# Optimization experiments

Hardware: AMD Instinct MI355X
Metric: run time of the kernel (lower is better)

## Reference

```python
import jax, jax.numpy as jnp
import numpy as np

B, W_DIM, CIN, COUT, K, H = 16, 512, 512, 512, 3, 64
PAD = (K - 1) // 2          # conv padding, also filtered_lrelu padding
GAIN = float(np.sqrt(2.0))  # lrelu gain (not torgb)
SLOPE = 0.2                 # lrelu slope (not torgb)
CLAMP = 256.0               # conv_clamp
AFFINE_WG = float(1.0 / np.sqrt(W_DIM))  # FullyConnectedLayer weight_gain


def setup_inputs() -> dict:
    key = jax.random.key(0)
    k0, k1, k2, k3 = jax.random.split(key, 4)
    return {
        "x": jax.random.normal(k0, (B, CIN, H, H), jnp.float32),
        "w": jax.random.normal(k1, (B, W_DIM), jnp.float32),
        "affine_weight": jax.random.normal(k2, (CIN, W_DIM), jnp.float32),
        "affine_bias": jnp.ones((CIN,), jnp.float32),       # bias_init=1
        "conv_weight": jax.random.normal(k3, (COUT, CIN, K, K), jnp.float32),
        "bias": jnp.zeros((COUT,), jnp.float32),
        "magnitude_ema": jnp.ones((), jnp.float32),
    }


def reference(x, w, affine_weight, affine_bias, conv_weight, bias, magnitude_ema):
    input_gain = jax.lax.rsqrt(magnitude_ema)
    # --- affine (FullyConnectedLayer, linear act, lr_mult=1) ---
    s = w @ (affine_weight * AFFINE_WG).T + affine_bias          # [B, CIN]
    # --- modulated_conv2d with demodulation (is_torgb=False) ---
    wk = conv_weight * jax.lax.rsqrt(
        jnp.mean(jnp.square(conv_weight), axis=(1, 2, 3), keepdims=True))
    s = s * jax.lax.rsqrt(jnp.mean(jnp.square(s)))
    wb = wk[None] * s[:, None, :, None, None]                    # [B,COUT,CIN,K,K]
    dcoefs = jax.lax.rsqrt(jnp.sum(jnp.square(wb), axis=(2, 3, 4)) + 1e-8)  # [B,COUT]
    wb = wb * dcoefs[:, :, None, None, None] * input_gain
    # grouped conv: groups = batch, one weight set per sample
    xg = x.reshape(1, B * CIN, H, H)
    wg = wb.reshape(B * COUT, CIN, K, K)
    y = jax.lax.conv_general_dilated(
        xg, wg, window_strides=(1, 1), padding=[(PAD, PAD), (PAD, PAD)],
        dimension_numbers=("NCHW", "OIHW", "NCHW"), feature_group_count=B)
    y = y.reshape(B, COUT, H, H)
    # --- filtered_lrelu: up=down=1, fu=fd=None (identity FIR) ---
    # => bias add, zero-pad by `padding`, lrelu * gain, clamp
    y = y + bias[:, None, None]
    y = jnp.pad(y, ((0, 0), (0, 0), (PAD, PAD), (PAD, PAD)))
    y = jnp.where(y >= 0, y, y * SLOPE) * GAIN
    y = jnp.clip(y, -CLAMP, CLAMP)                               # [B,COUT,66,66]
    return y
```

## Files before the change

kernel.cpp:

```cpp
#include <hip/hip_runtime.h>

#define B_     16
#define WDIM   512
#define CIN_   512
#define COUT_  512
#define HH     64
#define KC     32
#define NCHUNK (CIN_/KC)
#define AFFINE_WG 0.044194173824159216f
#define GAIN_  1.4142135623730951f
#define CLAMP_ 256.0f

#define WBYTES 36864
#define XBYTES 42240

typedef __attribute__((ext_vector_type(4))) float f32x4;
typedef __attribute__((ext_vector_type(8))) short bf16x8;
typedef __attribute__((ext_vector_type(8))) unsigned short u16x8;

__device__ __forceinline__ unsigned short f2bf(float f) {
    union { float f; unsigned u; } un; un.f = f;
    unsigned u = un.u;
    u += 0x7FFFu + ((u >> 16) & 1u);
    return (unsigned short)(u >> 16);
}

__device__ __forceinline__ void gl_lds16(const void* g, void* l) {
    __builtin_amdgcn_global_load_lds(
        reinterpret_cast<const __attribute__((address_space(1))) unsigned int*>(
            reinterpret_cast<uintptr_t>(g)),
        reinterpret_cast<__attribute__((address_space(3))) unsigned int*>(
            reinterpret_cast<uintptr_t>(l)),
        16, 0, 0);
}


__global__ void k_affine(const float* __restrict__ w, const float* __restrict__ aw,
                         const float* __restrict__ ab, float* __restrict__ s,
                         float* __restrict__ part) {
    const int tid = threadIdx.x;
    const int b = blockIdx.x >> 1;
    const int c = ((blockIdx.x & 1) << 8) + tid;
    const f32x4* wr = (const f32x4*)(w + (size_t)b * WDIM);
    const f32x4* ar = (const f32x4*)(aw + (size_t)c * WDIM);
    float acc = 0.f;
    #pragma unroll 4
    for (int k = 0; k < WDIM / 4; ++k) {
        f32x4 a = ar[k], bb = wr[k];
        acc += a[0]*bb[0] + a[1]*bb[1] + a[2]*bb[2] + a[3]*bb[3];
    }
    float sv = acc * AFFINE_WG + ab[c];
    s[b * CIN_ + c] = sv;
    __shared__ float red[256];
    red[tid] = sv * sv;
    __syncthreads();
    for (int off = 128; off > 0; off >>= 1) {
        if (tid < off) red[tid] += red[tid + off];
        __syncthreads();
    }
    if (tid == 0) part[blockIdx.x] = red[0];
}

__global__ void k_wnorm(const float* __restrict__ cw, float* __restrict__ alpha,
                        float* __restrict__ Q) {
    const int o = blockIdx.x;
    const int tid = threadIdx.x;
    __shared__ float qsh[512];
    __shared__ float red[256];
    __shared__ float a_sh;
    float tot = 0.f;
    #pragma unroll
    for (int half = 0; half < 2; ++half) {
        const int c = tid + half * 256;
        const float* p = cw + ((size_t)o * 512 + c) * 9;
        float qs = 0.f;
        #pragma unroll
        for (int t = 0; t < 9; ++t) { float v = p[t]; qs += v * v; }
        qsh[c] = qs; tot += qs;
    }
    red[tid] = tot; __syncthreads();
    for (int off = 128; off > 0; off >>= 1) {
        if (tid < off) red[tid] += red[tid + off];
        __syncthreads();
    }
    if (tid == 0) { a_sh = rsqrtf(red[0] * (1.0f / 4608.0f)); alpha[o] = a_sh; }
    __syncthreads();
    const float a2 = a_sh * a_sh;
    Q[(size_t)o * 512 + tid]       = a2 * qsh[tid];
    Q[(size_t)o * 512 + tid + 256] = a2 * qsh[tid + 256];
}

__global__ void k_g(const float* __restrict__ s, const float* __restrict__ part,
                    const float* __restrict__ Q, const float* __restrict__ alpha,
                    const float* __restrict__ ema, float* __restrict__ g) {
    const int tid = threadIdx.x;
    const int b = blockIdx.x >> 1;
    const int o = ((blockIdx.x & 1) << 8) + tid;
    __shared__ float rs2_sh;
    if (tid == 0) {
        float t = 0.f;
        #pragma unroll
        for (int i = 0; i < 32; ++i) t += part[i];
        rs2_sh = 8192.0f / t;
    }
    __syncthreads();
    const f32x4* sh = (const f32x4*)(s + (size_t)b * CIN_);
    const f32x4* qq = (const f32x4*)(Q + (size_t)o * CIN_);
    float d = 0.f;
    #pragma unroll 4
    for (int k = 0; k < CIN_ / 4; ++k) {
        f32x4 a = sh[k], q4 = qq[k];
        d += a[0]*a[0]*q4[0] + a[1]*a[1]*q4[1] + a[2]*a[2]*q4[2] + a[3]*a[3]*q4[3];
    }
    const float ig = rsqrtf(ema[0]);
    g[b * COUT_ + o] = alpha[o] * rsqrtf(d * rs2_sh + 1e-8f) * ig;
}

__global__ void k_wprep2(const float* __restrict__ cw, unsigned short* __restrict__ wb) {
    const int S = blockIdx.x * 256 + threadIdx.x;
    const int p    = S / 2304;
    const int srem = S - p * 2304;
    const int a    = srem * 16;
    const int tap  = a >> 12;
    const int o    = (a >> 6) & 63;
    const int c0   = ((a & 63) ^ ((o & 6) << 3)) >> 1;
    const int ot = p >> 4, cc = p & 15;
    const int og = ot * 64 + o;
    const int cg = cc * 32 + c0;
    const float* src = cw + ((size_t)og * 512 + cg) * 9 + tap;
    u16x8 v;
    #pragma unroll
    for (int j = 0; j < 8; ++j) v[j] = f2bf(src[j * 9]);
    *(u16x8*)(wb + (size_t)S * 8) = v;
}

__global__ void k_xprep2(const float* __restrict__ x, const float* __restrict__ s,
                         const float* __restrict__ part, unsigned short* __restrict__ xbf) {
    __shared__ float rs_sh;
    __shared__ char tile[8 * 4096];
    const int tid = threadIdx.x;
    if (tid == 0) {
        float t = 0.f;
        #pragma unroll
        for (int i = 0; i < 32; ++i) t += part[i];
        rs_sh = rsqrtf(t * (1.0f / 8192.0f));
    }
    __syncthreads();
    const float rs = rs_sh;
    const int blk = blockIdx.x;
    const int b  = blk >> 7;
    const int cc = (blk >> 3) & 15;
    const int rg = blk & 7;
    const int c   = tid >> 3;
    const int k8  = tid & 7;
    const float sc = s[b * CIN_ + cc * 32 + c] * rs;
    const float* src = x + (((size_t)(b * CIN_ + cc * 32 + c)) * HH + rg * 8) * HH + k8 * 8;
    #pragma unroll
    for (int row = 0; row < 8; ++row) {
        const f32x4 v0 = *(const f32x4*)(src + (size_t)row * HH);
        const f32x4 v1 = *(const f32x4*)(src + (size_t)row * HH + 4);
        #pragma unroll
        for (int q = 0; q < 8; ++q) {
            const float v = (q < 4) ? v0[q] : v1[q - 4];
            const int col = k8 * 8 + q + 1;
            const int byte = ((col * 64 + 2 * c) ^ ((col & 6) << 3)) - 64;
            *(unsigned short*)(tile + row * 4096 + byte) = f2bf(v * sc);
        }
    }
    __syncthreads();
    unsigned short* dst = xbf + ((size_t)(b * 16 + cc) * 64 + rg * 8) * 2048;
    const u16x8* tsrc = (const u16x8*)tile;
    #pragma unroll
    for (int k = 0; k < 8; ++k)
        *(u16x8*)(dst + (size_t)(tid + k * 256) * 8) = tsrc[tid + k * 256];
}

__global__ __launch_bounds__(512, 1) void k_conv4(
    const unsigned short* __restrict__ xbf, const unsigned short* __restrict__ wb,
    const float* __restrict__ g, const float* __restrict__ bias,
    float* __restrict__ out) {
    __shared__ char bufA[WBYTES + XBYTES];
    __shared__ char bufB[WBYTES + XBYTES];

    const int tid  = threadIdx.x;
    const int lane = tid & 63;
    const int wv   = tid >> 6;
    const int l15  = lane & 15;
    const int hi   = lane >> 4;

    const int orig = blockIdx.x;
    const int wg = (orig & 7) * 128 + (orig >> 3);
    const int b  = wg >> 6;
    const int ot = (wg >> 3) & 7;
    const int rt = wg & 7;
    const int h0 = rt * 8;

    const f32x4 zero4 = {0.f, 0.f, 0.f, 0.f};
    f32x4 acc[4][4];
    #pragma unroll
    for (int i = 0; i < 4; ++i)
        #pragma unroll
        for (int j = 0; j < 4; ++j) acc[i][j] = zero4;

    {
        unsigned int* x0 = (unsigned int*)(bufA + WBYTES);
        unsigned int* x1 = (unsigned int*)(bufB + WBYTES);
        for (int i = tid; i < XBYTES / 4; i += 512) { x0[i] = 0u; x1[i] = 0u; }
    }
    __syncthreads();

    const char* wsrc0 = (const char*)wb + (size_t)ot * 16 * WBYTES;
    const char* xsrc0 = (const char*)xbf + (size_t)b * 16 * 262144;

    auto STAGE = [&](char* base, int cc) {
        if (tid < 256) {
            const char* wsrc = wsrc0 + (size_t)cc * WBYTES;
            #pragma unroll
            for (int r = 0; r < 9; ++r)
                gl_lds16(wsrc + r * 4096 + tid * 16, base + r * 4096 + tid * 16);
        } else {
            const int t2 = tid - 256;
            const char* xsrc = xsrc0 + (size_t)cc * 262144;
            char* xb = base + WBYTES;
            #pragma unroll
            for (int r = 0; r < 10; ++r) {
                const int h_in = h0 - 1 + r;
                if ((unsigned)h_in < 64u)
                    gl_lds16(xsrc + (size_t)h_in * 4096 + t2 * 16,
                             xb + r * 4224 + 64 + t2 * 16);
            }
        }
    };

    auto COMPUTE = [&](const char* Wl, const char* Xl) {
        #pragma unroll
        for (int tap = 0; tap < 9; ++tap) {
            const int ti = tap / 3, tj = tap - ti * 3;
            bf16x8 af[4];
            #pragma unroll
            for (int mi = 0; mi < 4; ++mi) {
                const int o = mi * 16 + l15;
                int byte = (tap << 12) + (o << 6) + (hi << 4);
                byte ^= ((o & 6) << 3);
                af[mi] = *(const bf16x8*)(Wl + byte);
            }
            bf16x8 bg[4];
            const int row = wv + ti;
            #pragma unroll
            for (int ni = 0; ni < 4; ++ni) {
                const int col = ni * 16 + l15 + tj;
                int byte = (((row * 66 + col) << 5) + (hi << 3)) << 1;
                byte ^= ((col & 6) << 3);
                bg[ni] = *(const bf16x8*)(Xl + byte);
            }
            if (tap == 5) __builtin_amdgcn_s_barrier();
            __builtin_amdgcn_s_setprio(1);
            #pragma unroll
            for (int mi = 0; mi < 4; ++mi)
                #pragma unroll
                for (int ni = 0; ni < 4; ++ni)
                    acc[mi][ni] = __builtin_amdgcn_mfma_f32_16x16x32_bf16(
                        af[mi], bg[ni], acc[mi][ni], 0, 0, 0);
            __builtin_amdgcn_s_setprio(0);
        }
    };

    STAGE(bufA, 0);
    __syncthreads();

    #pragma unroll 1
    for (int it = 0; it < 8; ++it) {
        const int cc = it * 2;
        STAGE(bufB, cc + 1);
        COMPUTE(bufA, bufA + WBYTES);
        __syncthreads();
        if (cc + 2 < NCHUNK) STAGE(bufA, cc + 2);
        COMPUTE(bufB, bufB + WBYTES);
        __syncthreads();
    }

    {
        const int obase = ot * 64;
        const int orow = h0 + wv + 1;
        #pragma unroll
        for (int mi = 0; mi < 4; ++mi) {
            #pragma unroll
            for (int r = 0; r < 4; ++r) {
                const int o = obase + mi * 16 + hi * 4 + r;
                const float gg = g[b * COUT_ + o];
                const float bb = bias[o];
                float* op = out + ((size_t)(b * COUT_ + o) * 66 + orow) * 66;
                #pragma unroll
                for (int ni = 0; ni < 4; ++ni) {
                    float v = acc[mi][ni][r] * gg + bb;
                    v = (v >= 0.f ? v : v * 0.2f) * GAIN_;
                    v = fminf(fmaxf(v, -CLAMP_), CLAMP_);
                    op[ni * 16 + l15 + 1] = v;
                }
                if (l15 == 0)  op[0]  = 0.f;
                if (l15 == 15) op[65] = 0.f;
            }
        }
        if (rt == 0 || rt == 7) {
            const int row = (rt == 0) ? 0 : 65;
            for (int i = tid; i < 64 * 66; i += 512) {
                const int o = obase + i / 66, col = i - (i / 66) * 66;
                out[((size_t)(b * COUT_ + o) * 66 + row) * 66 + col] = 0.f;
            }
        }
    }
}

extern "C" void kernel_launch(void* const* d_in, const int* in_sizes, int n_in,
                              void* d_out, int out_size, void* d_ws, size_t ws_size,
                              hipStream_t stream) {
    const float* x    = (const float*)d_in[0];
    const float* w    = (const float*)d_in[1];
    const float* aw   = (const float*)d_in[2];
    const float* ab   = (const float*)d_in[3];
    const float* cw   = (const float*)d_in[4];
    const float* bias = (const float*)d_in[5];
    const float* ema  = (const float*)d_in[6];
    float* out = (float*)d_out;

    float* wsf   = (float*)d_ws;
    float* s     = wsf;
    float* part  = wsf + 8192;
    float* alpha = wsf + 16512;
    float* Q     = wsf + 17024;
    float* g     = wsf + 279168;
    unsigned short* wb  = (unsigned short*)((char*)d_ws + 1179648);
    unsigned short* xbf = (unsigned short*)((char*)d_ws + 5898240);

    k_affine <<<32, 256, 0, stream>>>(w, aw, ab, s, part);
    k_wnorm  <<<512, 256, 0, stream>>>(cw, alpha, Q);
    k_g      <<<32, 256, 0, stream>>>(s, part, Q, alpha, ema, g);
    k_wprep2 <<<1152, 256, 0, stream>>>(cw, wb);
    k_xprep2 <<<2048, 256, 0, stream>>>(x, s, part, xbf);
    k_conv4  <<<1024, 512, 0, stream>>>(xbf, wb, g, bias, out);
}
```

Before: 342.1 us.

## Replace double-buffered 512-thread conv with single-buffer 256-thread, 2-blocks-per-CU conv

The conv kernel moves from 512 threads with two LDS buffers and software double-buffering to 256 threads with a single LDS buffer and two output rows per wave. The intent is to run two blocks per CU so that one block's loads overlap with the other's MFMA work, in place of the explicit intra-block pipeline, while also reusing each loaded weight fragment across two rows. The cost is twice the accumulator registers per thread (128 floats of acc) and the loss of explicit prefetch. Load-to-compute overlap now depends on the other block sharing the CU.

```diff
diff --git a/kernel.cpp b/kernel.cpp
--- a/kernel.cpp
+++ b/kernel.cpp
@@ -175,12 +175,12 @@
         *(u16x8*)(dst + (size_t)(tid + k * 256) * 8) = tsrc[tid + k * 256];
 }
 
-__global__ __launch_bounds__(512, 1) void k_conv4(
+__global__ __launch_bounds__(256, 2) void k_conv5(
     const unsigned short* __restrict__ xbf, const unsigned short* __restrict__ wb,
     const float* __restrict__ g, const float* __restrict__ bias,
     float* __restrict__ out) {
-    __shared__ char bufA[WBYTES + XBYTES];
-    __shared__ char bufB[WBYTES + XBYTES];
+    __shared__ char Wl[WBYTES];
+    __shared__ char Xl[XBYTES];
 
     const int tid  = threadIdx.x;
     const int lane = tid & 63;
@@ -196,43 +196,41 @@
     const int h0 = rt * 8;
 
     const f32x4 zero4 = {0.f, 0.f, 0.f, 0.f};
-    f32x4 acc[4][4];
-    #pragma unroll
-    for (int i = 0; i < 4; ++i)
-        #pragma unroll
-        for (int j = 0; j < 4; ++j) acc[i][j] = zero4;
+    f32x4 acc[2][4][4];
+    #pragma unroll
+    for (int rr = 0; rr < 2; ++rr)
+        #pragma unroll
+        for (int i = 0; i < 4; ++i)
+            #pragma unroll
+            for (int j = 0; j < 4; ++j) acc[rr][i][j] = zero4;
 
     {
-        unsigned int* x0 = (unsigned int*)(bufA + WBYTES);
-        unsigned int* x1 = (unsigned int*)(bufB + WBYTES);
-        for (int i = tid; i < XBYTES / 4; i += 512) { x0[i] = 0u; x1[i] = 0u; }
+        unsigned int* x0 = (unsigned int*)Xl;
+        for (int i = tid; i < XBYTES / 4; i += 256) x0[i] = 0u;
     }
     __syncthreads();
 
     const char* wsrc0 = (const char*)wb + (size_t)ot * 16 * WBYTES;
     const char* xsrc0 = (const char*)xbf + (size_t)b * 16 * 262144;
 
-    auto STAGE = [&](char* base, int cc) {
-        if (tid < 256) {
+    #pragma unroll 1
+    for (int cc = 0; cc < NCHUNK; ++cc) {
+        {
             const char* wsrc = wsrc0 + (size_t)cc * WBYTES;
             #pragma unroll
             for (int r = 0; r < 9; ++r)
-                gl_lds16(wsrc + r * 4096 + tid * 16, base + r * 4096 + tid * 16);
-        } else {
-            const int t2 = tid - 256;
+                gl_lds16(wsrc + r * 4096 + tid * 16, Wl + r * 4096 + tid * 16);
             const char* xsrc = xsrc0 + (size_t)cc * 262144;
-            char* xb = base + WBYTES;
             #pragma unroll
             for (int r = 0; r < 10; ++r) {
                 const int h_in = h0 - 1 + r;
                 if ((unsigned)h_in < 64u)
-                    gl_lds16(xsrc + (size_t)h_in * 4096 + t2 * 16,
-                             xb + r * 4224 + 64 + t2 * 16);
-            }
-        }
-    };
-
-    auto COMPUTE = [&](const char* Wl, const char* Xl) {
+                    gl_lds16(xsrc + (size_t)h_in * 4096 + tid * 16,
+                             Xl + r * 4224 + 64 + tid * 16);
+            }
+        }
+        __syncthreads();
+
         #pragma unroll
         for (int tap = 0; tap < 9; ++tap) {
             const int ti = tap / 3, tj = tap - ti * 3;
@@ -244,66 +242,60 @@
                 byte ^= ((o & 6) << 3);
                 af[mi] = *(const bf16x8*)(Wl + byte);
             }
-            bf16x8 bg[4];
-            const int row = wv + ti;
-            #pragma unroll
-            for (int ni = 0; ni < 4; ++ni) {
-                const int col = ni * 16 + l15 + tj;
-                int byte = (((row * 66 + col) << 5) + (hi << 3)) << 1;
-                byte ^= ((col & 6) << 3);
-                bg[ni] = *(const bf16x8*)(Xl + byte);
-            }
-            if (tap == 5) __builtin_amdgcn_s_barrier();
+            bf16x8 bg[2][4];
+            #pragma unroll
+            for (int rr = 0; rr < 2; ++rr) {
+                const int row = 2 * wv + rr + ti;
+                #pragma unroll
+                for (int ni = 0; ni < 4; ++ni) {
+                    const int col = ni * 16 + l15 + tj;
+                    int byte = (((row * 66 + col) << 5) + (hi << 3)) << 1;
+                    byte ^= ((col & 6) << 3);
+                    bg[rr][ni] = *(const bf16x8*)(Xl + byte);
+                }
+            }
             __builtin_amdgcn_s_setprio(1);
             #pragma unroll
-            for (int mi = 0; mi < 4; ++mi)
+            for (int rr = 0; rr < 2; ++rr)
                 #pragma unroll
-                for (int ni = 0; ni < 4; ++ni)
-                    acc[mi][ni] = __builtin_amdgcn_mfma_f32_16x16x32_bf16(
-                        af[mi], bg[ni], acc[mi][ni], 0, 0, 0);
+                for (int mi = 0; mi < 4; ++mi)
+                    #pragma unroll
+                    for (int ni = 0; ni < 4; ++ni)
+                        acc[rr][mi][ni] = __builtin_amdgcn_mfma_f32_16x16x32_bf16(
+                            af[mi], bg[rr][ni], acc[rr][mi][ni], 0, 0, 0);
             __builtin_amdgcn_s_setprio(0);
         }
-    };
-
-    STAGE(bufA, 0);
-    __syncthreads();
-
-    #pragma unroll 1
-    for (int it = 0; it < 8; ++it) {
-        const int cc = it * 2;
-        STAGE(bufB, cc + 1);
-        COMPUTE(bufA, bufA + WBYTES);
-        __syncthreads();
-        if (cc + 2 < NCHUNK) STAGE(bufA, cc + 2);
-        COMPUTE(bufB, bufB + WBYTES);
-        __syncthreads();
+        if (cc != NCHUNK - 1) __syncthreads();
     }
 
     {
         const int obase = ot * 64;
-        const int orow = h0 + wv + 1;
-        #pragma unroll
-        for (int mi = 0; mi < 4; ++mi) {
-            #pragma unroll
-            for (int r = 0; r < 4; ++r) {
-                const int o = obase + mi * 16 + hi * 4 + r;
-                const float gg = g[b * COUT_ + o];
-                const float bb = bias[o];
-                float* op = out + ((size_t)(b * COUT_ + o) * 66 + orow) * 66;
+        #pragma unroll
+        for (int rr = 0; rr < 2; ++rr) {
+            const int orow = h0 + 2 * wv + rr + 1;
+            #pragma unroll
+            for (int mi = 0; mi < 4; ++mi) {
                 #pragma unroll
-                for (int ni = 0; ni < 4; ++ni) {
-                    float v = acc[mi][ni][r] * gg + bb;
-                    v = (v >= 0.f ? v : v * 0.2f) * GAIN_;
-                    v = fminf(fmaxf(v, -CLAMP_), CLAMP_);
-                    op[ni * 16 + l15 + 1] = v;
+                for (int r = 0; r < 4; ++r) {
+                    const int o = obase + mi * 16 + hi * 4 + r;
+                    const float gg = g[b * COUT_ + o];
+                    const float bb = bias[o];
+                    float* op = out + ((size_t)(b * COUT_ + o) * 66 + orow) * 66;
+                    #pragma unroll
+                    for (int ni = 0; ni < 4; ++ni) {
+                        float v = acc[rr][mi][ni][r] * gg + bb;
+                        v = (v >= 0.f ? v : v * 0.2f) * GAIN_;
+                        v = fminf(fmaxf(v, -CLAMP_), CLAMP_);
+                        op[ni * 16 + l15 + 1] = v;
+                    }
+                    if (l15 == 0)  op[0]  = 0.f;
+                    if (l15 == 15) op[65] = 0.f;
                 }
-                if (l15 == 0)  op[0]  = 0.f;
-                if (l15 == 15) op[65] = 0.f;
             }
         }
         if (rt == 0 || rt == 7) {
             const int row = (rt == 0) ? 0 : 65;
-            for (int i = tid; i < 64 * 66; i += 512) {
+            for (int i = tid; i < 64 * 66; i += 256) {
                 const int o = obase + i / 66, col = i - (i / 66) * 66;
                 out[((size_t)(b * COUT_ + o) * 66 + row) * 66 + col] = 0.f;
             }
@@ -337,5 +329,5 @@
     k_g      <<<32, 256, 0, stream>>>(s, part, Q, alpha, ema, g);
     k_wprep2 <<<1152, 256, 0, stream>>>(cw, wb);
     k_xprep2 <<<2048, 256, 0, stream>>>(x, s, part, xbf);
-    k_conv4  <<<1024, 512, 0, stream>>>(xbf, wb, g, bias, out);
-}
+    k_conv5  <<<1024, 256, 0, stream>>>(xbf, wb, g, bias, out);
+}
```

After: 337.7 us. Within noise of the previous version (-1.3%).

## Use counted vmcnt waits with explicit barriers in conv double-buffer pipeline

Applied to the files above, without the earlier changes.

The conv kernel's staging loop now has each thread issue the same number of global-to-LDS loads every stage, sending out-of-range halo rows to a dump buffer. That fixed count lets it wait with a counted s_waitcnt vmcnt instead of a full drain, so the next chunk's loads stay in flight while the current chunk is computed. Full __syncthreads are replaced by raw s_barrier calls fenced with sched_barrier, and the mid-compute barrier is removed. The cost is extra wasted loads for boundary rows, plus fragile hand-tuned wait counts that depend on how many loads each wave issues.

```diff
diff --git a/kernel.cpp b/kernel.cpp
--- a/kernel.cpp
+++ b/kernel.cpp
@@ -13,6 +13,7 @@
 
 #define WBYTES 36864
 #define XBYTES 42240
+#define BUFBYTES (WBYTES + XBYTES)
 
 typedef __attribute__((ext_vector_type(4))) float f32x4;
 typedef __attribute__((ext_vector_type(8))) short bf16x8;
@@ -175,12 +176,13 @@
         *(u16x8*)(dst + (size_t)(tid + k * 256) * 8) = tsrc[tid + k * 256];
 }
 
-__global__ __launch_bounds__(512, 1) void k_conv4(
+__global__ __launch_bounds__(512, 1) void k_conv7(
     const unsigned short* __restrict__ xbf, const unsigned short* __restrict__ wb,
     const float* __restrict__ g, const float* __restrict__ bias,
     float* __restrict__ out) {
-    __shared__ char bufA[WBYTES + XBYTES];
-    __shared__ char bufB[WBYTES + XBYTES];
+    __shared__ char bufA[BUFBYTES];
+    __shared__ char bufB[BUFBYTES];
+    __shared__ char dump[4096];
 
     const int tid  = threadIdx.x;
     const int lane = tid & 63;
@@ -225,11 +227,32 @@
             #pragma unroll
             for (int r = 0; r < 10; ++r) {
                 const int h_in = h0 - 1 + r;
-                if ((unsigned)h_in < 64u)
-                    gl_lds16(xsrc + (size_t)h_in * 4096 + t2 * 16,
-                             xb + r * 4224 + 64 + t2 * 16);
-            }
-        }
+                const bool ok = (unsigned)h_in < 64u;
+                const int hc = ok ? h_in : 0;
+                char* dst = ok ? (xb + r * 4224 + 64 + t2 * 16) : (dump + t2 * 16);
+                gl_lds16(xsrc + (size_t)hc * 4096 + t2 * 16, dst);
+            }
+        }
+    };
+
+    auto WAIT_PREV_BAR = [&]() {
+        if (wv < 4) asm volatile("s_waitcnt vmcnt(9)" ::: "memory");
+        else        asm volatile("s_waitcnt vmcnt(10)" ::: "memory");
+        __builtin_amdgcn_sched_barrier(0);
+        __builtin_amdgcn_s_barrier();
+        __builtin_amdgcn_sched_barrier(0);
+    };
+    auto WAIT0_BAR = [&]() {
+        asm volatile("s_waitcnt vmcnt(0)" ::: "memory");
+        __builtin_amdgcn_sched_barrier(0);
+        __builtin_amdgcn_s_barrier();
+        __builtin_amdgcn_sched_barrier(0);
+    };
+    auto POST_BAR = [&]() {
+        asm volatile("" ::: "memory");
+        __builtin_amdgcn_sched_barrier(0);
+        __builtin_amdgcn_s_barrier();
+        __builtin_amdgcn_sched_barrier(0);
     };
 
     auto COMPUTE = [&](const char* Wl, const char* Xl) {
@@ -253,7 +276,6 @@
                 byte ^= ((col & 6) << 3);
                 bg[ni] = *(const bf16x8*)(Xl + byte);
             }
-            if (tap == 5) __builtin_amdgcn_s_barrier();
             __builtin_amdgcn_s_setprio(1);
             #pragma unroll
             for (int mi = 0; mi < 4; ++mi)
@@ -266,18 +288,26 @@
     };
 
     STAGE(bufA, 0);
-    __syncthreads();
+    WAIT0_BAR();
 
     #pragma unroll 1
-    for (int it = 0; it < 8; ++it) {
+    for (int it = 0; it < 7; ++it) {
         const int cc = it * 2;
         STAGE(bufB, cc + 1);
+        WAIT_PREV_BAR();
         COMPUTE(bufA, bufA + WBYTES);
-        __syncthreads();
-        if (cc + 2 < NCHUNK) STAGE(bufA, cc + 2);
+        POST_BAR();
+        STAGE(bufA, cc + 2);
+        WAIT_PREV_BAR();
         COMPUTE(bufB, bufB + WBYTES);
-        __syncthreads();
-    }
+        POST_BAR();
+    }
+    STAGE(bufB, 15);
+    WAIT_PREV_BAR();
+    COMPUTE(bufA, bufA + WBYTES);
+    POST_BAR();
+    WAIT0_BAR();
+    COMPUTE(bufB, bufB + WBYTES);
 
     {
         const int obase = ot * 64;
@@ -337,5 +367,5 @@
     k_g      <<<32, 256, 0, stream>>>(s, part, Q, alpha, ema, g);
     k_wprep2 <<<1152, 256, 0, stream>>>(cw, wb);
     k_xprep2 <<<2048, 256, 0, stream>>>(x, s, part, xbf);
-    k_conv4  <<<1024, 512, 0, stream>>>(xbf, wb, g, bias, out);
-}
+    k_conv7  <<<1024, 512, 0, stream>>>(xbf, wb, g, bias, out);
+}
```

Result: slower. 349.5 us (+2.2%).

## Single-buffer conv LDS staging to raise occupancy to multiple blocks per CU

Applied to the files above, without the earlier changes.

Replaces the double-buffered LDS pipeline in the conv kernel with a single W/X buffer that is loaded, synchronised and then computed once per channel chunk. Launch bounds move from 1 to 4 blocks per CU. The goal is to roughly halve LDS use so more blocks fit per CU and other blocks hide load latency, in place of in-block prefetch overlap. The cost is that each block now stalls on every chunk's global loads, and register pressure under the tighter launch bounds may cause spills.

```diff
diff --git a/kernel.cpp b/kernel.cpp
--- a/kernel.cpp
+++ b/kernel.cpp
@@ -12,7 +12,8 @@
 #define CLAMP_ 256.0f
 
 #define WBYTES 36864
-#define XBYTES 42240
+#define XROWB  4224
+#define XBYTES (10 * XROWB)
 
 typedef __attribute__((ext_vector_type(4))) float f32x4;
 typedef __attribute__((ext_vector_type(8))) short bf16x8;
@@ -175,12 +176,12 @@
         *(u16x8*)(dst + (size_t)(tid + k * 256) * 8) = tsrc[tid + k * 256];
 }
 
-__global__ __launch_bounds__(512, 1) void k_conv4(
+__global__ __launch_bounds__(512, 4) void k_conv9(
     const unsigned short* __restrict__ xbf, const unsigned short* __restrict__ wb,
     const float* __restrict__ g, const float* __restrict__ bias,
     float* __restrict__ out) {
-    __shared__ char bufA[WBYTES + XBYTES];
-    __shared__ char bufB[WBYTES + XBYTES];
+    __shared__ char Wl[WBYTES];
+    __shared__ char Xl[XBYTES];
 
     const int tid  = threadIdx.x;
     const int lane = tid & 63;
@@ -203,36 +204,34 @@
         for (int j = 0; j < 4; ++j) acc[i][j] = zero4;
 
     {
-        unsigned int* x0 = (unsigned int*)(bufA + WBYTES);
-        unsigned int* x1 = (unsigned int*)(bufB + WBYTES);
-        for (int i = tid; i < XBYTES / 4; i += 512) { x0[i] = 0u; x1[i] = 0u; }
+        unsigned int* x0 = (unsigned int*)Xl;
+        for (int i = tid; i < XBYTES / 4; i += 512) x0[i] = 0u;
     }
     __syncthreads();
 
     const char* wsrc0 = (const char*)wb + (size_t)ot * 16 * WBYTES;
     const char* xsrc0 = (const char*)xbf + (size_t)b * 16 * 262144;
 
-    auto STAGE = [&](char* base, int cc) {
+    #pragma unroll 1
+    for (int cc = 0; cc < NCHUNK; ++cc) {
         if (tid < 256) {
             const char* wsrc = wsrc0 + (size_t)cc * WBYTES;
             #pragma unroll
             for (int r = 0; r < 9; ++r)
-                gl_lds16(wsrc + r * 4096 + tid * 16, base + r * 4096 + tid * 16);
+                gl_lds16(wsrc + r * 4096 + tid * 16, Wl + r * 4096 + tid * 16);
         } else {
             const int t2 = tid - 256;
             const char* xsrc = xsrc0 + (size_t)cc * 262144;
-            char* xb = base + WBYTES;
             #pragma unroll
             for (int r = 0; r < 10; ++r) {
                 const int h_in = h0 - 1 + r;
                 if ((unsigned)h_in < 64u)
                     gl_lds16(xsrc + (size_t)h_in * 4096 + t2 * 16,
-                             xb + r * 4224 + 64 + t2 * 16);
-            }
-        }
-    };
-
-    auto COMPUTE = [&](const char* Wl, const char* Xl) {
+                             Xl + r * XROWB + 64 + t2 * 16);
+            }
+        }
+        __syncthreads();
+
         #pragma unroll
         for (int tap = 0; tap < 9; ++tap) {
             const int ti = tap / 3, tj = tap - ti * 3;
@@ -253,7 +252,6 @@
                 byte ^= ((col & 6) << 3);
                 bg[ni] = *(const bf16x8*)(Xl + byte);
             }
-            if (tap == 5) __builtin_amdgcn_s_barrier();
             __builtin_amdgcn_s_setprio(1);
             #pragma unroll
             for (int mi = 0; mi < 4; ++mi)
@@ -263,20 +261,7 @@
                         af[mi], bg[ni], acc[mi][ni], 0, 0, 0);
             __builtin_amdgcn_s_setprio(0);
         }
-    };
-
-    STAGE(bufA, 0);
-    __syncthreads();
-
-    #pragma unroll 1
-    for (int it = 0; it < 8; ++it) {
-        const int cc = it * 2;
-        STAGE(bufB, cc + 1);
-        COMPUTE(bufA, bufA + WBYTES);
-        __syncthreads();
-        if (cc + 2 < NCHUNK) STAGE(bufA, cc + 2);
-        COMPUTE(bufB, bufB + WBYTES);
-        __syncthreads();
+        if (cc != NCHUNK - 1) __syncthreads();
     }
 
     {
@@ -337,5 +322,5 @@
     k_g      <<<32, 256, 0, stream>>>(s, part, Q, alpha, ema, g);
     k_wprep2 <<<1152, 256, 0, stream>>>(cw, wb);
     k_xprep2 <<<2048, 256, 0, stream>>>(x, s, part, xbf);
-    k_conv4  <<<1024, 512, 0, stream>>>(xbf, wb, g, bias, out);
-}
+    k_conv9  <<<1024, 512, 0, stream>>>(xbf, wb, g, bias, out);
+}
```

After: 499.1 us. 1.46x slower.
